# Performance work log

Hardware: AMD Instinct MI355X
Metric: run time of the kernel (lower is better)

## Reference

```python
import jax, jax.numpy as jnp
import numpy as np

N_SRC, N_TGT, E = 50000, 10000, 150000
D_IN, D_OUT = 512, 512
N_ETYPES, N_NTYPES = 8, 4


def setup_inputs() -> dict:
    key = jax.random.key(0)
    ks = jax.random.split(key, 9)
    scale = 1.0 / np.sqrt(D_IN)
    return {
        "x_src": jax.random.normal(ks[0], (N_SRC, D_IN), jnp.float32),
        "x_target": jax.random.normal(ks[1], (N_TGT, D_IN), jnp.float32),
        "rel_W": jax.random.normal(ks[2], (N_ETYPES, D_IN, D_OUT), jnp.float32) * scale,
        "root_W": jax.random.normal(ks[3], (N_NTYPES, D_IN, D_OUT), jnp.float32) * scale,
        "root_b": jax.random.normal(ks[4], (N_NTYPES, D_OUT), jnp.float32) * scale,
        "edge_src": jax.random.randint(ks[5], (E,), 0, N_SRC, jnp.int64).astype(jnp.int32),
        "edge_dst": jax.random.randint(ks[6], (E,), 0, N_TGT, jnp.int64).astype(jnp.int32),
        "edge_type": jax.random.randint(ks[7], (E,), 0, N_ETYPES, jnp.int64).astype(jnp.int32),
        "target_node_type": jax.random.randint(ks[8], (N_TGT,), 0, N_NTYPES, jnp.int64).astype(jnp.int32),
    }


def reference(x_src, x_target, rel_W, root_W, root_b,
              edge_src, edge_dst, edge_type, target_node_type):
    T = rel_W.shape[0]
    n_tgt = x_target.shape[0]
    # Transform every source node under every relation (grouped GEMM),
    # then gather per edge: msg_e = W_{etype_e} @ x_src[src_e].
    h = jnp.einsum('ni,tio->tno', x_src, rel_W)          # [T, N_src, D_out]
    msg = h[edge_type, edge_src]                          # [E, D_out]
    # PyG aggr='mean' is applied per edge type then SUMMED across types:
    # segment-mean keyed by (dst, etype), empty segments contribute 0.
    seg = edge_dst * T + edge_type                        # [E]
    sums = jax.ops.segment_sum(msg, seg, num_segments=n_tgt * T)
    counts = jax.ops.segment_sum(jnp.ones((msg.shape[0],), msg.dtype), seg,
                                 num_segments=n_tgt * T)
    means = sums / jnp.maximum(counts, 1.0)[:, None]      # [N_tgt*T, D_out]
    out = means.reshape(n_tgt, T, -1).sum(axis=1)         # [N_tgt, D_out]
    # Per-node-type root linear (with bias), selected per target node.
    root = jnp.einsum('ni,tio->nto', x_target, root_W) + root_b[None]  # [N_tgt, NT, D_out]
    root_sel = jnp.take_along_axis(root, target_node_type[:, None, None], axis=1)[:, 0]
    return out + root_sel
```

## Files before the change

kernel.cpp:

```cpp
#include <hip/hip_runtime.h>
#include <hip/hip_bf16.h>

#define D 512
#define T_ETYPES 8
#define NT_TYPES 4
#define K_MAIN 4096
#define K_A 4608
#define K_B 6144
#define SPLITS 6
#define KSPLIT 768

typedef __attribute__((ext_vector_type(8))) short bf16x8;
typedef __attribute__((ext_vector_type(4))) float f32x4;

__device__ __forceinline__ unsigned short f2bf(float f) {
    union { float f; unsigned u; } u{f};
    unsigned r = u.u + 0x7FFF + ((u.u >> 16) & 1);
    return (unsigned short)(r >> 16);
}
__device__ __forceinline__ float bf2f(unsigned short h) {
    union { unsigned u; float f; } v{(unsigned)h << 16};
    return v.f;
}

__device__ __forceinline__ void gl16(const unsigned short* g, unsigned short* l) {
    __builtin_amdgcn_global_load_lds(
        (const __attribute__((address_space(1))) unsigned int*)g,
        (__attribute__((address_space(3))) unsigned int*)l,
        16, 0, 0);
}

__global__ void convert_weights(const float* __restrict__ relW,
                                const float* __restrict__ rootW,
                                unsigned short* __restrict__ WbT) {
    __shared__ float tile[32][33];
    int c0 = blockIdx.x * 32;
    int o0 = blockIdx.y * 32;
    int tid = threadIdx.x;
#pragma unroll
    for (int it = 0; it < 4; ++it) {
        int idx = it * 256 + tid;
        int oc = idx & 31, cc = idx >> 5;
        int c = c0 + cc, o = o0 + oc;
        float v = (c < K_MAIN) ? relW[(size_t)c * D + o]
                               : rootW[(size_t)(c - K_MAIN) * D + o];
        tile[cc][oc] = v;
    }
    __syncthreads();
#pragma unroll
    for (int it = 0; it < 4; ++it) {
        int idx = it * 256 + tid;
        int cc = idx & 31, oc = idx >> 5;
        WbT[(size_t)(o0 + oc) * K_B + (c0 + cc)] = f2bf(tile[cc][oc]);
    }
}

__global__ void hist_kernel(const int* __restrict__ edst, const int* __restrict__ etyp,
                            int* __restrict__ counts, int E) {
    int e = blockIdx.x * 256 + threadIdx.x;
    if (e < E) atomicAdd(&counts[edst[e] * T_ETYPES + etyp[e]], 1);
}

__global__ void scan1(const int* __restrict__ counts, int* __restrict__ partial,
                      int* __restrict__ blockSums, int n) {
    __shared__ int sh[256];
    int tid = threadIdx.x, i = blockIdx.x * 256 + tid;
    int c = (i < n) ? counts[i] : 0;
    int val = c;
    sh[tid] = val; __syncthreads();
#pragma unroll
    for (int off = 1; off < 256; off <<= 1) {
        int add = (tid >= off) ? sh[tid - off] : 0;
        __syncthreads();
        val += add; sh[tid] = val;
        __syncthreads();
    }
    if (i < n) partial[i] = val - c;
    if (tid == 255) blockSums[blockIdx.x] = val;
}

__global__ void scan2(int* __restrict__ blockSums, int nb) {
    __shared__ int sh[512];
    int tid = threadIdx.x;
    int c = (tid < nb) ? blockSums[tid] : 0;
    int val = c;
    sh[tid] = val; __syncthreads();
#pragma unroll
    for (int off = 1; off < 512; off <<= 1) {
        int add = (tid >= off) ? sh[tid - off] : 0;
        __syncthreads();
        val += add; sh[tid] = val;
        __syncthreads();
    }
    if (tid < nb) blockSums[tid] = val - c;
}

__global__ void scan3(const int* __restrict__ partial, const int* __restrict__ blockSums,
                      int* __restrict__ offsets, int* __restrict__ cursors, int n) {
    int i = blockIdx.x * 256 + threadIdx.x;
    if (i < n) {
        int v = partial[i] + blockSums[i >> 8];
        offsets[i] = v;
        cursors[i] = v;
    }
}

__global__ void scatter_kernel(const int* __restrict__ esrc, const int* __restrict__ edst,
                               const int* __restrict__ etyp, int* __restrict__ cursors,
                               int* __restrict__ perm, int E) {
    int e = blockIdx.x * 256 + threadIdx.x;
    if (e < E) {
        int seg = edst[e] * T_ETYPES + etyp[e];
        int pos = atomicAdd(&cursors[seg], 1);
        perm[pos] = esrc[e];
    }
}

__global__ void thist2(const int* __restrict__ tnt, int* __restrict__ bcnt, int M) {
    __shared__ int h[NT_TYPES];
    if (threadIdx.x < NT_TYPES) h[threadIdx.x] = 0;
    __syncthreads();
    int i = blockIdx.x * 256 + threadIdx.x;
    if (i < M) atomicAdd(&h[tnt[i]], 1);
    __syncthreads();
    if (threadIdx.x < NT_TYPES) bcnt[blockIdx.x * NT_TYPES + threadIdx.x] = h[threadIdx.x];
}

__global__ void tprep2(const int* __restrict__ bcnt, int nb,
                       int* __restrict__ boff, int* __restrict__ gstart,
                       int* __restrict__ endv) {
    __shared__ int sb[128 * NT_TYPES];
    __shared__ int gs[NT_TYPES];
    int tid = threadIdx.x;
    for (int i = tid; i < nb * NT_TYPES; i += blockDim.x) sb[i] = bcnt[i];
    __syncthreads();
    if (tid == 0) {
        int s = 0;
        for (int g = 0; g < NT_TYPES; ++g) {
            int tot = 0;
            for (int b = 0; b < nb; ++b) tot += sb[b * NT_TYPES + g];
            gs[g] = s;
            gstart[g] = s;
            endv[g] = s + tot;
            s += ((tot + 127) >> 7) << 7;
        }
        gstart[NT_TYPES] = s;
    }
    __syncthreads();
    if (tid < NT_TYPES) {
        int run = gs[tid];
        for (int b = 0; b < nb; ++b) {
            boff[b * NT_TYPES + tid] = run;
            run += sb[b * NT_TYPES + tid];
        }
    }
}

__global__ void tscatter2(const int* __restrict__ tnt, const int* __restrict__ boff,
                          int* __restrict__ rowperm, int* __restrict__ invperm, int M) {
    __shared__ int h[NT_TYPES];
    if (threadIdx.x < NT_TYPES) h[threadIdx.x] = 0;
    __syncthreads();
    int n = blockIdx.x * 256 + threadIdx.x;
    if (n < M) {
        int g = tnt[n];
        int lr = atomicAdd(&h[g], 1);
        int p = boff[blockIdx.x * NT_TYPES + g] + lr;
        rowperm[p] = n;
        invperm[n] = p;
    }
}

__global__ void segmean(const float* __restrict__ x_src, const int* __restrict__ perm,
                        const int* __restrict__ offsets, const int* __restrict__ counts,
                        const int* __restrict__ invperm,
                        unsigned short* __restrict__ A, int nseg) {
    int seg = blockIdx.x * 4 + (threadIdx.x >> 6);
    if (seg >= nseg) return;
    int lane = threadIdx.x & 63;
    int beg = offsets[seg], cnt = counts[seg];
    float4 a0 = make_float4(0.f, 0.f, 0.f, 0.f);
    float4 a1 = make_float4(0.f, 0.f, 0.f, 0.f);
    for (int i = 0; i < cnt; ++i) {
        int s = perm[beg + i];
        const float4* p = reinterpret_cast<const float4*>(x_src + (size_t)s * D);
        float4 v0 = p[lane * 2], v1 = p[lane * 2 + 1];
        a0.x += v0.x; a0.y += v0.y; a0.z += v0.z; a0.w += v0.w;
        a1.x += v1.x; a1.y += v1.y; a1.z += v1.z; a1.w += v1.w;
    }
    float sc = (cnt > 0) ? 1.0f / (float)cnt : 0.0f;
    uint4 u;
    u.x = (unsigned)f2bf(a0.x * sc) | ((unsigned)f2bf(a0.y * sc) << 16);
    u.y = (unsigned)f2bf(a0.z * sc) | ((unsigned)f2bf(a0.w * sc) << 16);
    u.z = (unsigned)f2bf(a1.x * sc) | ((unsigned)f2bf(a1.y * sc) << 16);
    u.w = (unsigned)f2bf(a1.z * sc) | ((unsigned)f2bf(a1.w * sc) << 16);
    int dst = seg >> 3, t = seg & 7;
    int nrow = invperm[dst];
    *reinterpret_cast<uint4*>(A + (size_t)nrow * K_A + t * D + lane * 8) = u;
}

__global__ void rootfill(const float* __restrict__ x_target, const int* __restrict__ invperm,
                         unsigned short* __restrict__ A, int M) {
    int idx = blockIdx.x * 256 + threadIdx.x;
    if (idx >= M * 64) return;
    int n = idx >> 6;
    int col = (idx & 63) * 8;
    const float4* p = reinterpret_cast<const float4*>(x_target + (size_t)n * D + col);
    float4 v0 = p[0], v1 = p[1];
    uint4 u;
    u.x = (unsigned)f2bf(v0.x) | ((unsigned)f2bf(v0.y) << 16);
    u.y = (unsigned)f2bf(v0.z) | ((unsigned)f2bf(v0.w) << 16);
    u.z = (unsigned)f2bf(v1.x) | ((unsigned)f2bf(v1.y) << 16);
    u.w = (unsigned)f2bf(v1.z) | ((unsigned)f2bf(v1.w) << 16);
    *reinterpret_cast<uint4*>(A + (size_t)invperm[n] * K_A + K_MAIN + col) = u;
}

__global__ __launch_bounds__(256, 4)
void rgcn_gemm_sk(const unsigned short* __restrict__ A,
                  const unsigned short* __restrict__ WbT,
                  unsigned short* __restrict__ pbuf,
                  const int* __restrict__ gstart, const int* __restrict__ endv,
                  int MBP, int MPc) {
    __shared__ unsigned short As[128 * 32];
    __shared__ unsigned short Bs[128 * 32];
    const int tid = threadIdx.x;

    int d = blockIdx.x;
    int l = d;
    if ((gridDim.x & 7) == 0) {
        int cpx = gridDim.x >> 3;
        l = (d & 7) * cpx + (d >> 3);
    }
    const int nIdx = l & 3;
    const int mz = l >> 2;
    const int mIdx = mz % MBP;
    const int zIdx = mz / MBP;

    const int blockM = mIdx * 128;
    const int blockN = nIdx * 128;
    const int kBase = zIdx * KSPLIT;
    const int g = (blockM >= gstart[1]) + (blockM >= gstart[2]) + (blockM >= gstart[3]);
    const int endRow = endv[g];
    const int rootOff = g * 512;

    const int wid = tid >> 6, lane = tid & 63;
    const int wr = wid >> 1, wc = wid & 1;
    const int lr = lane & 15, lg = lane >> 4;

    f32x4 acc[4][4] = {};

    const int c0 = tid, c1 = 256 + tid;
    const unsigned short* Abase = A + (size_t)blockM * K_A + kBase;
    const unsigned short* Bbase = WbT + (size_t)blockN * K_B;

    for (int t = 0; t < KSPLIT / 32; ++t) {
        const int k0 = t * 32;
        const int kc = kBase + k0;
        const int bc = (kc < K_MAIN) ? kc : kc + rootOff;
        gl16(Abase + (size_t)(c0 >> 2) * K_A + k0 + (c0 & 3) * 8, &As[c0 * 8]);
        gl16(Abase + (size_t)(c1 >> 2) * K_A + k0 + (c1 & 3) * 8, &As[c1 * 8]);
        gl16(Bbase + (size_t)(c0 >> 2) * K_B + bc + (c0 & 3) * 8, &Bs[c0 * 8]);
        gl16(Bbase + (size_t)(c1 >> 2) * K_B + bc + (c1 & 3) * 8, &Bs[c1 * 8]);
        __syncthreads();

        bf16x8 a_frag[4], b_frag[4];
#pragma unroll
        for (int mi = 0; mi < 4; ++mi)
            a_frag[mi] = *reinterpret_cast<const bf16x8*>(&As[(wr * 64 + mi * 16 + lr) * 32 + lg * 8]);
#pragma unroll
        for (int ni = 0; ni < 4; ++ni)
            b_frag[ni] = *reinterpret_cast<const bf16x8*>(&Bs[(wc * 64 + ni * 16 + lr) * 32 + lg * 8]);
#pragma unroll
        for (int mi = 0; mi < 4; ++mi)
#pragma unroll
            for (int ni = 0; ni < 4; ++ni)
                acc[mi][ni] = __builtin_amdgcn_mfma_f32_16x16x32_bf16(a_frag[mi], b_frag[ni], acc[mi][ni], 0, 0, 0);
        __syncthreads();
    }

#pragma unroll
    for (int mi = 0; mi < 4; ++mi) {
#pragma unroll
        for (int r = 0; r < 4; ++r) {
            int row = blockM + wr * 64 + mi * 16 + lg * 4 + r;
            if (row < endRow) {
#pragma unroll
                for (int ni = 0; ni < 4; ++ni) {
                    int col = blockN + wc * 64 + ni * 16 + lr;
                    pbuf[((size_t)zIdx * MPc + row) * D + col] = f2bf(acc[mi][ni][r]);
                }
            }
        }
    }
}

__global__ void reduce_bias(const unsigned short* __restrict__ pbuf,
                            const int* __restrict__ rowperm, const int* __restrict__ tnt,
                            const float* __restrict__ root_b,
                            float* __restrict__ out, int MPc) {
    int idx = blockIdx.x * 256 + threadIdx.x;
    if (idx >= MPc * 64) return;
    int nrow = idx >> 6;
    int col = (idx & 63) * 8;
    int orig = rowperm[nrow];
    if (orig < 0) return;
    float s[8] = {0.f, 0.f, 0.f, 0.f, 0.f, 0.f, 0.f, 0.f};
#pragma unroll
    for (int sp = 0; sp < SPLITS; ++sp) {
        uint4 v = *reinterpret_cast<const uint4*>(pbuf + ((size_t)sp * MPc + nrow) * D + col);
        unsigned u[4] = {v.x, v.y, v.z, v.w};
#pragma unroll
        for (int j = 0; j < 4; ++j) {
            s[2 * j]     += bf2f((unsigned short)(u[j] & 0xFFFF));
            s[2 * j + 1] += bf2f((unsigned short)(u[j] >> 16));
        }
    }
    const float* b = root_b + (size_t)tnt[orig] * D + col;
    float4 o0, o1;
    o0.x = s[0] + b[0]; o0.y = s[1] + b[1]; o0.z = s[2] + b[2]; o0.w = s[3] + b[3];
    o1.x = s[4] + b[4]; o1.y = s[5] + b[5]; o1.z = s[6] + b[6]; o1.w = s[7] + b[7];
    float* o = out + (size_t)orig * D + col;
    *reinterpret_cast<float4*>(o) = o0;
    *reinterpret_cast<float4*>(o + 4) = o1;
}

extern "C" void kernel_launch(void* const* d_in, const int* in_sizes, int n_in,
                              void* d_out, int out_size, void* d_ws, size_t ws_size,
                              hipStream_t stream) {
    const float* x_src    = (const float*)d_in[0];
    const float* x_target = (const float*)d_in[1];
    const float* relW     = (const float*)d_in[2];
    const float* rootW    = (const float*)d_in[3];
    const float* rootb    = (const float*)d_in[4];
    const int*   esrc     = (const int*)d_in[5];
    const int*   edst     = (const int*)d_in[6];
    const int*   etyp     = (const int*)d_in[7];
    const int*   tnt      = (const int*)d_in[8];
    float* out = (float*)d_out;

    const int E = in_sizes[5];
    const int M = in_sizes[8];
    const int NSEG = M * T_ETYPES;
    const int NB = (NSEG + 255) / 256;
    const int NBT = (M + 255) / 256;
    const int MBP = (M + 127) / 128 + (NT_TYPES - 1);
    const int MPc = MBP * 128;

    char* ws = (char*)d_ws;
    size_t off = 0;
    unsigned short* Abf = (unsigned short*)(ws + off); off += (size_t)MPc * K_A * 2;
    unsigned short* WbT = (unsigned short*)(ws + off); off += (size_t)D * K_B * 2;
    unsigned short* pb  = (unsigned short*)(ws + off); off += (size_t)SPLITS * MPc * D * 2;
    int* counts    = (int*)(ws + off); off += (size_t)NSEG * 4;
    int* partial   = (int*)(ws + off); off += (size_t)NSEG * 4;
    int* offsets   = (int*)(ws + off); off += (size_t)NSEG * 4;
    int* cursors   = (int*)(ws + off); off += (size_t)NSEG * 4;
    int* blockSums = (int*)(ws + off); off += 512 * 4;
    int* perm      = (int*)(ws + off); off += (size_t)E * 4;
    int* bcnt      = (int*)(ws + off); off += (size_t)NBT * NT_TYPES * 4;
    int* boff      = (int*)(ws + off); off += (size_t)NBT * NT_TYPES * 4;
    int* gstart    = (int*)(ws + off); off += 8 * 4;
    int* endv      = (int*)(ws + off); off += 8 * 4;
    int* rowperm   = (int*)(ws + off); off += (size_t)MPc * 4;
    int* invperm   = (int*)(ws + off); off += (size_t)M * 4;

    hipMemsetAsync(counts, 0, (size_t)NSEG * 4, stream);
    hipMemsetAsync(rowperm, 0xFF, (size_t)MPc * 4, stream);

    convert_weights<<<dim3(K_B / 32, D / 32), 256, 0, stream>>>(relW, rootW, WbT);
    thist2<<<NBT, 256, 0, stream>>>(tnt, bcnt, M);
    tprep2<<<1, 256, 0, stream>>>(bcnt, NBT, boff, gstart, endv);
    tscatter2<<<NBT, 256, 0, stream>>>(tnt, boff, rowperm, invperm, M);
    hist_kernel<<<(E + 255) / 256, 256, 0, stream>>>(edst, etyp, counts, E);
    scan1<<<NB, 256, 0, stream>>>(counts, partial, blockSums, NSEG);
    scan2<<<1, 512, 0, stream>>>(blockSums, NB);
    scan3<<<NB, 256, 0, stream>>>(partial, blockSums, offsets, cursors, NSEG);
    scatter_kernel<<<(E + 255) / 256, 256, 0, stream>>>(esrc, edst, etyp, cursors, perm, E);
    segmean<<<(NSEG + 3) / 4, 256, 0, stream>>>(x_src, perm, offsets, counts, invperm, Abf, NSEG);
    rootfill<<<(M * 64 + 255) / 256, 256, 0, stream>>>(x_target, invperm, Abf, M);
    rgcn_gemm_sk<<<MBP * 4 * SPLITS, 256, 0, stream>>>(Abf, WbT, pb, gstart, endv, MBP, MPc);
    reduce_bias<<<(MPc * 64 + 255) / 256, 256, 0, stream>>>(pb, rowperm, tnt, rootb, out, MPc);
}
```

Before: 195.7 us.

## Pre-swizzle GEMM operands in global memory and double K-tile to 64

The producer kernels (weight transpose, segment-mean, root fill) now write the A and WbT operands with an XOR swizzle of 16-byte chunks within each 64-element K block, keyed on the row index. The GEMM stages a 64-wide K tile per barrier pair and reads fragments through the matching swizzle. This is meant to avoid LDS bank conflicts on the direct global-to-LDS loads without extra address math, and to halve the number of sync iterations. In exchange it doubles LDS use per block, which may reduce occupancy, and it couples every producer to the GEMM's internal layout.

Result: faster. 186.8 us (-4.5%).

```diff
diff --git a/kernel.cpp b/kernel.cpp
--- a/kernel.cpp
+++ b/kernel.cpp
@@ -9,6 +9,8 @@
 #define K_B 6144
 #define SPLITS 6
 #define KSPLIT 768
+#define BK 64
+
 
 typedef __attribute__((ext_vector_type(8))) short bf16x8;
 typedef __attribute__((ext_vector_type(4))) float f32x4;
@@ -51,7 +53,9 @@
     for (int it = 0; it < 4; ++it) {
         int idx = it * 256 + tid;
         int cc = idx & 31, oc = idx >> 5;
-        WbT[(size_t)(o0 + oc) * K_B + (c0 + cc)] = f2bf(tile[cc][oc]);
+        int o = o0 + oc, c = c0 + cc;
+        int csw = (c & ~63) | (((((c >> 3) & 7) ^ (o & 7))) << 3) | (c & 7);
+        WbT[(size_t)o * K_B + csw] = f2bf(tile[cc][oc]);
     }
 }
 
@@ -196,7 +200,8 @@
     u.w = (unsigned)f2bf(a1.z * sc) | ((unsigned)f2bf(a1.w * sc) << 16);
     int dst = seg >> 3, t = seg & 7;
     int nrow = invperm[dst];
-    *reinterpret_cast<uint4*>(A + (size_t)nrow * K_A + t * D + lane * 8) = u;
+    int col = t * D + ((lane >> 3) << 6) + (((lane & 7) ^ (nrow & 7)) << 3);
+    *reinterpret_cast<uint4*>(A + (size_t)nrow * K_A + col) = u;
 }
 
 __global__ void rootfill(const float* __restrict__ x_target, const int* __restrict__ invperm,
@@ -204,15 +209,17 @@
     int idx = blockIdx.x * 256 + threadIdx.x;
     if (idx >= M * 64) return;
     int n = idx >> 6;
-    int col = (idx & 63) * 8;
-    const float4* p = reinterpret_cast<const float4*>(x_target + (size_t)n * D + col);
+    int q = idx & 63;
+    const float4* p = reinterpret_cast<const float4*>(x_target + (size_t)n * D + q * 8);
     float4 v0 = p[0], v1 = p[1];
     uint4 u;
     u.x = (unsigned)f2bf(v0.x) | ((unsigned)f2bf(v0.y) << 16);
     u.y = (unsigned)f2bf(v0.z) | ((unsigned)f2bf(v0.w) << 16);
     u.z = (unsigned)f2bf(v1.x) | ((unsigned)f2bf(v1.y) << 16);
     u.w = (unsigned)f2bf(v1.z) | ((unsigned)f2bf(v1.w) << 16);
-    *reinterpret_cast<uint4*>(A + (size_t)invperm[n] * K_A + K_MAIN + col) = u;
+    int prow = invperm[n];
+    int col = K_MAIN + ((q >> 3) << 6) + (((q & 7) ^ (prow & 7)) << 3);
+    *reinterpret_cast<uint4*>(A + (size_t)prow * K_A + col) = u;
 }
 
 __global__ __launch_bounds__(256, 4)
@@ -221,8 +228,8 @@
                   unsigned short* __restrict__ pbuf,
                   const int* __restrict__ gstart, const int* __restrict__ endv,
                   int MBP, int MPc) {
-    __shared__ unsigned short As[128 * 32];
-    __shared__ unsigned short Bs[128 * 32];
+    __shared__ unsigned short As[128 * BK];
+    __shared__ unsigned short Bs[128 * BK];
     const int tid = threadIdx.x;
 
     int d = blockIdx.x;
@@ -249,32 +256,47 @@
 
     f32x4 acc[4][4] = {};
 
-    const int c0 = tid, c1 = 256 + tid;
     const unsigned short* Abase = A + (size_t)blockM * K_A + kBase;
     const unsigned short* Bbase = WbT + (size_t)blockN * K_B;
 
-    for (int t = 0; t < KSPLIT / 32; ++t) {
-        const int k0 = t * 32;
+    for (int t = 0; t < KSPLIT / BK; ++t) {
+        const int k0 = t * BK;
         const int kc = kBase + k0;
         const int bc = (kc < K_MAIN) ? kc : kc + rootOff;
-        gl16(Abase + (size_t)(c0 >> 2) * K_A + k0 + (c0 & 3) * 8, &As[c0 * 8]);
-        gl16(Abase + (size_t)(c1 >> 2) * K_A + k0 + (c1 & 3) * 8, &As[c1 * 8]);
-        gl16(Bbase + (size_t)(c0 >> 2) * K_B + bc + (c0 & 3) * 8, &Bs[c0 * 8]);
-        gl16(Bbase + (size_t)(c1 >> 2) * K_B + bc + (c1 & 3) * 8, &Bs[c1 * 8]);
-        __syncthreads();
-
-        bf16x8 a_frag[4], b_frag[4];
-#pragma unroll
-        for (int mi = 0; mi < 4; ++mi)
-            a_frag[mi] = *reinterpret_cast<const bf16x8*>(&As[(wr * 64 + mi * 16 + lr) * 32 + lg * 8]);
-#pragma unroll
-        for (int ni = 0; ni < 4; ++ni)
-            b_frag[ni] = *reinterpret_cast<const bf16x8*>(&Bs[(wc * 64 + ni * 16 + lr) * 32 + lg * 8]);
-#pragma unroll
-        for (int mi = 0; mi < 4; ++mi)
-#pragma unroll
-            for (int ni = 0; ni < 4; ++ni)
-                acc[mi][ni] = __builtin_amdgcn_mfma_f32_16x16x32_bf16(a_frag[mi], b_frag[ni], acc[mi][ni], 0, 0, 0);
+#pragma unroll
+        for (int q = 0; q < 4; ++q) {
+            int c = q * 256 + tid;
+            gl16(Abase + (size_t)(c >> 3) * K_A + k0 + (c & 7) * 8, &As[c * 8]);
+        }
+#pragma unroll
+        for (int q = 0; q < 4; ++q) {
+            int c = q * 256 + tid;
+            gl16(Bbase + (size_t)(c >> 3) * K_B + bc + (c & 7) * 8, &Bs[c * 8]);
+        }
+        __syncthreads();
+
+#pragma unroll
+        for (int ks = 0; ks < 2; ++ks) {
+            bf16x8 a_frag[4], b_frag[4];
+#pragma unroll
+            for (int mi = 0; mi < 4; ++mi) {
+                int r = wr * 64 + mi * 16 + lr;
+                a_frag[mi] = *reinterpret_cast<const bf16x8*>(
+                    &As[r * BK + (((ks * 4 + lg) ^ (r & 7)) << 3)]);
+            }
+#pragma unroll
+            for (int ni = 0; ni < 4; ++ni) {
+                int cR = wc * 64 + ni * 16 + lr;
+                b_frag[ni] = *reinterpret_cast<const bf16x8*>(
+                    &Bs[cR * BK + (((ks * 4 + lg) ^ (cR & 7)) << 3)]);
+            }
+#pragma unroll
+            for (int mi = 0; mi < 4; ++mi)
+#pragma unroll
+                for (int ni = 0; ni < 4; ++ni)
+                    acc[mi][ni] = __builtin_amdgcn_mfma_f32_16x16x32_bf16(
+                        a_frag[mi], b_frag[ni], acc[mi][ni], 0, 0, 0);
+        }
         __syncthreads();
     }
 
```
